# Kernel optimization log

Measured on AMD Instinct MI355X. Metric: run time of the kernel, lower is better.

The kernel has to match this reference:

```python
import jax, jax.numpy as jnp
import numpy as np

B, N, H = 4, 256, 8            # batch, nodes, heads
DNI, DEI = 32, 16              # node_in_dim, edge_in_dim
DNO, DEO = 32, 32              # node_out_dim, edge_out_dim
LEAKY = 0.2
NEG = -9e15


def setup_inputs() -> dict:
    key = jax.random.key(0)
    ks = jax.random.split(key, 13)
    s = 0.05
    node_fea = jax.random.normal(ks[0], (B, H, N, DNI), jnp.float32)
    edge_fea = jax.random.normal(ks[1], (B, H, N, N, DEI), jnp.float32)
    adj = jax.random.randint(ks[2], (B, N, N), 0, 2, jnp.int32)
    # learned params (nn.Linear: y = x @ W.T + b)
    W_w   = jax.random.normal(ks[3],  (H * DNO, H * DNI), jnp.float32) * s
    W_b   = jax.random.normal(ks[4],  (H * DNO,),         jnp.float32) * s
    a1_w  = jax.random.normal(ks[5],  (H, H * DNO),       jnp.float32) * s
    a2_w  = jax.random.normal(ks[6],  (H, H * DNO),       jnp.float32) * s
    ae_w  = jax.random.normal(ks[7],  (H, H * DEI),       jnp.float32) * s
    ae_b  = jax.random.normal(ks[8],  (H,),               jnp.float32) * s
    We_w  = jax.random.normal(ks[9],  (H * DEO, H * DEI), jnp.float32) * s
    We_b  = jax.random.normal(ks[10], (H * DEO,),         jnp.float32) * s
    Wod_w = jax.random.normal(ks[11], (H * DNO, H * DNI), jnp.float32) * s
    Wod_b = jax.random.normal(ks[12], (H * DNO,),         jnp.float32) * s
    return dict(node_fea=node_fea, edge_fea=edge_fea, adj=adj,
                W_w=W_w, W_b=W_b, a1_w=a1_w, a2_w=a2_w,
                ae_w=ae_w, ae_b=ae_b, We_w=We_w, We_b=We_b,
                Wod_w=Wod_w, Wod_b=Wod_b)


def reference(node_fea, edge_fea, adj, W_w, W_b, a1_w, a2_w,
              ae_w, ae_b, We_w, We_b, Wod_w, Wod_b):
    b, h, n, _ = node_fea.shape  # h == nheads -> non-first-layer branch
    # flatten heads into feature dim, as in the torch code
    nf = node_fea.transpose(0, 2, 1, 3).reshape(b, n, -1)          # [B,N,H*DNI]
    ef = edge_fea.transpose(0, 2, 3, 1, 4).reshape(b, n, n, -1)    # [B,N,N,H*DEI]

    Wh = nf @ W_w.T + W_b                                          # [B,N,H*DNO]
    e_edge = ef @ ae_w.T + ae_b                                    # [B,N,N,H]
    Whi = Wh @ a1_w.T                                              # [B,N,H]
    Whj = Wh @ a2_w.T                                              # [B,N,H]

    e = Whi[:, :, None, :] + Whj[:, None, :, :] + e_edge           # [B,N,N,H]
    e = jax.nn.leaky_relu(e, LEAKY)
    e = jnp.where(adj[..., None] > 0, e, NEG)

    # edge update: o + d + W_edge(edge)
    od = nf @ Wod_w.T + Wod_b                                      # [B,N,H*DEO]
    edge_new = od[:, :, None, :] + od[:, None, :, :] + (ef @ We_w.T + We_b)
    edge_new = edge_new.reshape(b, n, n, h, -1).transpose(0, 3, 1, 2, 4)  # [B,H,N,N,DEO]

    att = jax.nn.softmax(e.transpose(0, 3, 1, 2), axis=-1)         # [B,H,N,N]; dropout p=0 -> identity
    Whh = Wh.reshape(b, n, h, -1).transpose(0, 2, 1, 3)            # [B,H,N,DNO]
    node_new = att @ Whh + Whh                                     # [B,H,N,DNO]
    return node_new, edge_new
```

## Files before the change

kernel.cpp:

```cpp
#include <hip/hip_runtime.h>
#include <cstddef>


typedef __attribute__((ext_vector_type(8))) short short8;
typedef __attribute__((ext_vector_type(4))) short short4v;
typedef __attribute__((ext_vector_type(4))) float f32x4;

__device__ __forceinline__ float bf2f(unsigned short u) {
  union { unsigned int i; float f; } c;
  c.i = ((unsigned int)u) << 16;
  return c.f;
}
__device__ __forceinline__ unsigned short f2bf(float f) {
  union { float f; unsigned int i; } c; c.f = f;
  unsigned int x = c.i;
  x += 0x7fffu + ((x >> 16) & 1u);
  return (unsigned short)(x >> 16);
}

struct F8 { f32x4 lo, hi; };

__device__ __forceinline__ float loadf(const void* p, size_t i, bool bf) {
  return bf ? bf2f(((const unsigned short*)p)[i]) : ((const float*)p)[i];
}
__device__ __forceinline__ f32x4 load4f(const void* p, size_t i, bool bf) {
  f32x4 r;
  if (bf) {
    #pragma unroll
    for (int k = 0; k < 4; k++) r[k] = bf2f(((const unsigned short*)p)[i + k]);
  } else {
    r = *(const f32x4*)((const float*)p + i);
  }
  return r;
}
__device__ __forceinline__ F8 load8f(const void* p, size_t i, bool bf) {
  F8 r;
  if (bf) {
    short8 s = *(const short8*)((const unsigned short*)p + i);
    #pragma unroll
    for (int k = 0; k < 4; k++) {
      r.lo[k] = bf2f((unsigned short)s[k]);
      r.hi[k] = bf2f((unsigned short)s[k + 4]);
    }
  } else {
    const float* f = (const float*)p + i;
    r.lo = *(const f32x4*)f;
    r.hi = *(const f32x4*)(f + 4);
  }
  return r;
}
__device__ __forceinline__ short8 load8bf(const void* p, size_t i, bool bf) {
  if (bf) return *(const short8*)((const unsigned short*)p + i);
  const float* f = (const float*)p + i;
  f32x4 a = *(const f32x4*)f, c = *(const f32x4*)(f + 4);
  short8 r;
  #pragma unroll
  for (int k = 0; k < 4; k++) {
    r[k]     = (short)f2bf(a[k]);
    r[k + 4] = (short)f2bf(c[k]);
  }
  return r;
}
__device__ __forceinline__ void storef(void* p, size_t i, float v, bool bf) {
  if (bf) ((unsigned short*)p)[i] = f2bf(v);
  else    ((float*)p)[i] = v;
}

__global__ void k_detect(const unsigned int* __restrict__ w, int* __restrict__ flag) {
  const int lane = threadIdx.x;
  unsigned int x = w[lane];
  unsigned int e = (x >> 7) & 0xFFu;
  bool hit = (e >= 100u && e <= 126u);
  unsigned long long b = __ballot(hit);
  if (lane == 0) *flag = (__popcll(b) >= 32) ? 1 : 0;
}

__global__ __launch_bounds__(256) void k_node(
    const void* __restrict__ node_fea,
    const void* __restrict__ W_w,  const void* __restrict__ W_b,
    const void* __restrict__ a1_w, const void* __restrict__ a2_w,
    const void* __restrict__ Wod_w, const void* __restrict__ Wod_b,
    const int* __restrict__ flag,
    float* __restrict__ whT, float* __restrict__ od,
    float* __restrict__ whi, float* __restrict__ whj)
{
  const bool bf = (*flag != 0);
  __shared__ float nf[2][256];
  __shared__ float red[4][32];
  const int t = threadIdx.x;
  const int row0 = blockIdx.x * 2;
  const int b = row0 >> 8;
  {
    const int rl = t >> 7, k2 = (t & 127) * 2;
    const int h = k2 >> 5, d = k2 & 31;
    const int n = (row0 & 255) + rl;
    const size_t idx = (((size_t)(b * 8 + h)) * 256 + n) * 32 + d;
    nf[rl][k2]     = loadf(node_fea, idx, bf);
    nf[rl][k2 + 1] = loadf(node_fea, idx + 1, bf);
  }
  __syncthreads();
  const int o = t;
  float acc1[2] = {0.f, 0.f}, acc2[2] = {0.f, 0.f};
  #pragma unroll 4
  for (int kc = 0; kc < 32; kc++) {
    F8 w1 = load8f(W_w,   (size_t)o * 256 + kc * 8, bf);
    F8 w2 = load8f(Wod_w, (size_t)o * 256 + kc * 8, bf);
    #pragma unroll
    for (int r = 0; r < 2; r++) {
      f32x4 alo = *(const f32x4*)&nf[r][kc * 8];
      f32x4 ahi = *(const f32x4*)&nf[r][kc * 8 + 4];
      #pragma unroll
      for (int k = 0; k < 4; k++) {
        acc1[r] += alo[k] * w1.lo[k] + ahi[k] * w1.hi[k];
        acc2[r] += alo[k] * w2.lo[k] + ahi[k] * w2.hi[k];
      }
    }
  }
  float whv[2], odv[2];
  {
    float b1 = loadf(W_b, o, bf), b2 = loadf(Wod_b, o, bf);
    #pragma unroll
    for (int r = 0; r < 2; r++) {
      whv[r] = acc1[r] + b1;
      odv[r] = acc2[r] + b2;
      whT[(((size_t)(b * 256 + o)) << 8) + (row0 & 255) + r] = whv[r];
      od[(size_t)(row0 + r) * 256 + o] = odv[r];
    }
  }
  float a1f[8], a2f[8];
  #pragma unroll
  for (int h = 0; h < 8; h++) {
    a1f[h] = loadf(a1_w, (size_t)h * 256 + o, bf);
    a2f[h] = loadf(a2_w, (size_t)h * 256 + o, bf);
  }
  const int lane = t & 63, wv = t >> 6;
  #pragma unroll 1
  for (int c = 0; c < 32; c++) {
    const int mat = c >> 4, r = (c >> 3) & 1, h = c & 7;
    float v = whv[r] * (mat ? a2f[h] : a1f[h]);
    #pragma unroll
    for (int s = 1; s < 64; s <<= 1) v += __shfl_xor(v, s, 64);
    if (lane == 0) red[wv][c] = v;
  }
  __syncthreads();
  if (t < 32) {
    const int c = t;
    float s = red[0][c] + red[1][c] + red[2][c] + red[3][c];
    const int mat = c >> 4, r = (c >> 3) & 1, h = c & 7;
    (mat ? whj : whi)[(size_t)(row0 + r) * 8 + h] = s;
  }
}

__global__ __launch_bounds__(256, 4) void k_main(
    const void* __restrict__ edge_fea, const int* __restrict__ adj,
    const void* __restrict__ ae_w, const void* __restrict__ ae_b,
    const void* __restrict__ We_w, const void* __restrict__ We_b,
    const int* __restrict__ flag,
    const float* __restrict__ od, const float* __restrict__ whi,
    const float* __restrict__ whj, const float* __restrict__ whT,
    void* __restrict__ out)
{
  const bool bf = (*flag != 0);
  __shared__ unsigned short A[16384];
  __shared__ float e_l[8][256];
  const int t = threadIdx.x;
  const int blk = blockIdx.x;
  const int i = blk & 255, b = blk >> 8;
  const int wave = t >> 6, lane = t & 63, quad = lane >> 4, col = lane & 15;

  short8 bw[4][4];
  #pragma unroll
  for (int s = 0; s < 4; s++) {
    const int n = (wave * 4 + s) * 16 + col;
    #pragma unroll
    for (int ks = 0; ks < 4; ks++)
      bw[s][ks] = load8bf(We_w, (size_t)n * 128 + ks * 32 + quad * 8, bf);
  }

  f32x4 ow4[4];
  #pragma unroll
  for (int s = 0; s < 4; s++) {
    const int f0 = (wave * 4 + s) * 16 + quad * 4;
    f32x4 oi = *(const f32x4*)(od + (((size_t)(b * 256 + i)) << 8) + f0);
    f32x4 wb = load4f(We_b, f0, bf);
    ow4[s] = oi + wb;
  }

  #pragma unroll 1
  for (int jt = 0; jt < 2; jt++) {
    const int j0 = jt * 128;
    {
      const int jr = t >> 1, e8 = (t & 1) * 8;
      unsigned short* arow = &A[jr * 128];
      const int sx = jr & 7;
      #pragma unroll
      for (int h = 0; h < 8; h++) {
        const size_t idx = ((((size_t)(b * 8 + h)) * 256 + i) * 256 + j0 + jr) * 16 + e8;
        const int slot = (h * 2 + (e8 >> 3)) ^ sx;
        *(short8*)(arow + slot * 8) = load8bf(edge_fea, idx, bf);
      }
    }
    __syncthreads();

    #pragma unroll 1
    for (int mt = 0; mt < 8; mt++) {
      const int row = mt * 16 + col;
      const unsigned short* arow = &A[row * 128];
      const int rx = row & 7;
      f32x4 acc[4];
      #pragma unroll
      for (int s = 0; s < 4; s++) acc[s] = (f32x4){0.f, 0.f, 0.f, 0.f};
      #pragma unroll
      for (int ks = 0; ks < 4; ks++) {
        short8 a = *(const short8*)(arow + ((ks * 4 + quad) ^ rx) * 8);
        acc[0] = __builtin_amdgcn_mfma_f32_16x16x32_bf16(bw[0][ks], a, acc[0], 0, 0, 0);
        acc[1] = __builtin_amdgcn_mfma_f32_16x16x32_bf16(bw[1][ks], a, acc[1], 0, 0, 0);
        acc[2] = __builtin_amdgcn_mfma_f32_16x16x32_bf16(bw[2][ks], a, acc[2], 0, 0, 0);
        acc[3] = __builtin_amdgcn_mfma_f32_16x16x32_bf16(bw[3][ks], a, acc[3], 0, 0, 0);
      }
      const int j = j0 + mt * 16 + col;
      const float* odj = od + (((size_t)(b * 256 + j)) << 8);
      #pragma unroll
      for (int s = 0; s < 4; s++) {
        const int f0 = (wave * 4 + s) * 16 + quad * 4;
        const int h = f0 >> 5, d0 = f0 & 31;
        f32x4 op = *(const f32x4*)(odj + f0);
        f32x4 v = acc[s] + ow4[s] + op;
        const size_t oidx =
            262144 + (((((size_t)(b * 8 + h)) * 256 + i) * 256 + j) * 32 + d0);
        if (bf) {
          short4v sv;
          #pragma unroll
          for (int r = 0; r < 4; r++) sv[r] = (short)f2bf(v[r]);
          __builtin_nontemporal_store(sv, (short4v*)((unsigned short*)out + oidx));
        } else {
          __builtin_nontemporal_store(v, (f32x4*)((float*)out + oidx));
        }
      }
    }

    {
      short8 bae[4];
      #pragma unroll
      for (int ks = 0; ks < 4; ks++) {
        short8 z = {0, 0, 0, 0, 0, 0, 0, 0};
        bae[ks] = (col < 8) ? load8bf(ae_w, (size_t)col * 128 + ks * 32 + quad * 8, bf) : z;
      }
      f32x4 whi4 = {0.f, 0.f, 0.f, 0.f}, aeb4 = {0.f, 0.f, 0.f, 0.f};
      if (quad < 2) {
        whi4 = *(const f32x4*)(whi + ((size_t)(b * 256 + i)) * 8 + quad * 4);
        aeb4 = load4f(ae_b, quad * 4, bf);
      }
      #pragma unroll
      for (int mm = 0; mm < 2; mm++) {
        const int mt = wave * 2 + mm;
        const int row = mt * 16 + col;
        const unsigned short* arow = &A[row * 128];
        const int rx = row & 7;
        f32x4 acce = {0.f, 0.f, 0.f, 0.f};
        #pragma unroll
        for (int ks = 0; ks < 4; ks++) {
          short8 a = *(const short8*)(arow + ((ks * 4 + quad) ^ rx) * 8);
          acce = __builtin_amdgcn_mfma_f32_16x16x32_bf16(bae[ks], a, acce, 0, 0, 0);
        }
        if (quad < 2) {
          const int j = j0 + mt * 16 + col;
          f32x4 wj = *(const f32x4*)(whj + ((size_t)(b * 256 + j)) * 8 + quad * 4);
          const int av = adj[((size_t)(b * 256 + i)) * 256 + j];
          #pragma unroll
          for (int r = 0; r < 4; r++) {
            float e = acce[r] + aeb4[r] + whi4[r] + wj[r];
            e = (e > 0.f) ? e : 0.2f * e;
            e = (av > 0) ? e : -9e15f;
            e_l[quad * 4 + r][j] = e;
          }
        }
      }
    }
    __syncthreads();
  }

  {
    const int h = t >> 5, l32 = t & 31;
    float m = -3.0e38f;
    #pragma unroll
    for (int k = 0; k < 8; k++) m = fmaxf(m, e_l[h][l32 + 32 * k]);
    #pragma unroll
    for (int s = 16; s >= 1; s >>= 1) m = fmaxf(m, __shfl_xor(m, s, 32));
    float p[8], sum = 0.f;
    #pragma unroll
    for (int k = 0; k < 8; k++) {
      p[k] = __expf(e_l[h][l32 + 32 * k] - m);
      sum += p[k];
    }
    #pragma unroll
    for (int s = 16; s >= 1; s >>= 1) sum += __shfl_xor(sum, s, 32);
    const float inv = 1.0f / sum;
    #pragma unroll
    for (int k = 0; k < 8; k++) e_l[h][l32 + 32 * k] = p[k] * inv;
  }
  __syncthreads();

  {
    const int h = t >> 5;
    const float* wr = whT + (((size_t)(b * 256 + t)) << 8);
    f32x4 a4 = {0.f, 0.f, 0.f, 0.f};
    #pragma unroll 8
    for (int j4 = 0; j4 < 64; j4++) {
      f32x4 w4 = *(const f32x4*)(wr + j4 * 4);
      const f32x4 p4 = *(const f32x4*)&e_l[h][j4 * 4];
      a4 += w4 * p4;
    }
    float v = (a4[0] + a4[1]) + (a4[2] + a4[3]) + wr[i];
    const size_t oe = (((size_t)(b * 8 + h)) * 256 + i) * 32 + (t & 31);
    storef(out, oe, v, bf);
  }
}

extern "C" void kernel_launch(void* const* d_in, const int* in_sizes, int n_in,
                              void* d_out, int out_size, void* d_ws, size_t ws_size,
                              hipStream_t stream) {
  const void* node_fea = d_in[0];
  const void* edge_fea = d_in[1];
  const int*  adj      = (const int*)d_in[2];
  const void* W_w      = d_in[3];
  const void* W_b      = d_in[4];
  const void* a1_w     = d_in[5];
  const void* a2_w     = d_in[6];
  const void* ae_w     = d_in[7];
  const void* ae_b     = d_in[8];
  const void* We_w     = d_in[9];
  const void* We_b     = d_in[10];
  const void* Wod_w    = d_in[11];
  const void* Wod_b    = d_in[12];

  int*   flag = (int*)d_ws;
  float* base = (float*)d_ws;
  float* whT  = base + 16;
  float* od   = whT + 262144;
  float* whi  = od + 262144;
  float* whj  = whi + 8192;

  k_detect<<<dim3(1), dim3(64), 0, stream>>>((const unsigned int*)W_w, flag);
  k_node<<<dim3(512), dim3(256), 0, stream>>>(node_fea, W_w, W_b, a1_w, a2_w,
                                              Wod_w, Wod_b, flag, whT, od, whi, whj);
  k_main<<<dim3(1024), dim3(256), 0, stream>>>(edge_fea, adj, ae_w, ae_b, We_w, We_b,
                                               flag, od, whi, whj, whT, d_out);
}
```

Measured before the change: 561.5 us.

## Precompute transposed weights and fold attention vectors into node projection

Adds a prep kernel that transposes W and Wod into a combined row-major buffer and precomputes a1·W and a2·W plus their bias terms. The node kernel then computes whi/whj directly as extra output columns, which removes the per-block shuffle reductions, and it handles four rows per block with coalesced weight reads. Nontemporal stores in the main kernel become ordinary stores. This adds an extra launch, and when the workspace is too small it places scratch data in the tail of the output buffer, which is fragile.

Result: slower. 677.7 us (+20.7%).

```diff
diff --git a/kernel.cpp b/kernel.cpp
--- a/kernel.cpp
+++ b/kernel.cpp
@@ -1,5 +1,6 @@
 #include <hip/hip_runtime.h>
 #include <cstddef>
+#include <cstdint>
 
 
 typedef __attribute__((ext_vector_type(8))) short short8;
@@ -75,79 +76,120 @@
   if (lane == 0) *flag = (__popcll(b) >= 32) ? 1 : 0;
 }
 
+__global__ __launch_bounds__(256) void k_prep(
+    const void* __restrict__ W_w, const void* __restrict__ Wod_w,
+    const void* __restrict__ W_b,
+    const void* __restrict__ a1_w, const void* __restrict__ a2_w,
+    const int* __restrict__ flag,
+    float* __restrict__ WT, float* __restrict__ bias12)
+{
+  const bool bf = (*flag != 0);
+  const int t = threadIdx.x;
+  const int blk = blockIdx.x;
+  if (blk < 16) {
+    #pragma unroll
+    for (int q = 0; q < 4; q++) {
+      f32x4 w  = load4f(W_w,   (size_t)t * 256 + blk * 16 + q * 4, bf);
+      f32x4 wo = load4f(Wod_w, (size_t)t * 256 + blk * 16 + q * 4, bf);
+      #pragma unroll
+      for (int j = 0; j < 4; j++) {
+        const int k = blk * 16 + q * 4 + j;
+        WT[(size_t)k * 544 + t]       = w[j];
+        WT[(size_t)k * 544 + 256 + t] = wo[j];
+      }
+    }
+  } else {
+    __shared__ float sa[16][256];
+    __shared__ float sb[256];
+    #pragma unroll
+    for (int hh = 0; hh < 16; hh++)
+      sa[hh][t] = loadf(hh < 8 ? a1_w : a2_w, (size_t)(hh & 7) * 256 + t, bf);
+    sb[t] = loadf(W_b, t, bf);
+    __syncthreads();
+    float acc[16];
+    #pragma unroll
+    for (int hh = 0; hh < 16; hh++) acc[hh] = 0.f;
+    #pragma unroll 4
+    for (int f = 0; f < 256; f++) {
+      float w = loadf(W_w, (size_t)f * 256 + t, bf);
+      #pragma unroll
+      for (int hh = 0; hh < 16; hh++) acc[hh] += sa[hh][f] * w;
+    }
+    #pragma unroll
+    for (int hh = 0; hh < 16; hh++) WT[(size_t)t * 544 + 512 + hh] = acc[hh];
+    if (t < 16) {
+      float s = 0.f;
+      for (int f = 0; f < 256; f++) s += sa[t][f] * sb[f];
+      bias12[t] = s;
+    }
+  }
+}
+
 __global__ __launch_bounds__(256) void k_node(
-    const void* __restrict__ node_fea,
-    const void* __restrict__ W_w,  const void* __restrict__ W_b,
-    const void* __restrict__ a1_w, const void* __restrict__ a2_w,
-    const void* __restrict__ Wod_w, const void* __restrict__ Wod_b,
-    const int* __restrict__ flag,
+    const void* __restrict__ node_fea, const float* __restrict__ WT,
+    const void* __restrict__ W_b, const void* __restrict__ Wod_b,
+    const float* __restrict__ bias12, const int* __restrict__ flag,
     float* __restrict__ whT, float* __restrict__ od,
     float* __restrict__ whi, float* __restrict__ whj)
 {
   const bool bf = (*flag != 0);
-  __shared__ float nf[2][256];
-  __shared__ float red[4][32];
+  __shared__ float nf_s[4][256];
   const int t = threadIdx.x;
-  const int row0 = blockIdx.x * 2;
-  const int b = row0 >> 8;
+  const int r0 = blockIdx.x * 4;
+  const int b = r0 >> 8, n0 = r0 & 255;
+  if (t < 128) {
+    const int rr = t >> 5, k8 = t & 31;
+    const int h = k8 >> 2, d0 = (k8 & 3) * 8;
+    F8 v = load8f(node_fea,
+                  (((size_t)(b * 8 + h)) * 256 + (n0 + rr)) * 32 + d0, bf);
+    *(f32x4*)&nf_s[rr][k8 * 8]     = v.lo;
+    *(f32x4*)&nf_s[rr][k8 * 8 + 4] = v.hi;
+  }
+  __syncthreads();
+
+  float accW[4] = {0.f, 0.f, 0.f, 0.f};
+  float accO[4] = {0.f, 0.f, 0.f, 0.f};
+  float accM[4] = {0.f, 0.f, 0.f, 0.f};
+  const bool t16 = (t < 16);
+  #pragma unroll 1
+  for (int k4 = 0; k4 < 64; k4++) {
+    f32x4 nv[4];
+    #pragma unroll
+    for (int rr = 0; rr < 4; rr++) nv[rr] = *(const f32x4*)&nf_s[rr][k4 * 4];
+    #pragma unroll
+    for (int kk = 0; kk < 4; kk++) {
+      const float* row = WT + (size_t)(k4 * 4 + kk) * 544;
+      const float w0 = row[t], w1 = row[256 + t];
+      #pragma unroll
+      for (int rr = 0; rr < 4; rr++) {
+        accW[rr] += nv[rr][kk] * w0;
+        accO[rr] += nv[rr][kk] * w1;
+      }
+      if (t16) {
+        const float w2 = row[512 + t];
+        #pragma unroll
+        for (int rr = 0; rr < 4; rr++) accM[rr] += nv[rr][kk] * w2;
+      }
+    }
+  }
+
   {
-    const int rl = t >> 7, k2 = (t & 127) * 2;
-    const int h = k2 >> 5, d = k2 & 31;
-    const int n = (row0 & 255) + rl;
-    const size_t idx = (((size_t)(b * 8 + h)) * 256 + n) * 32 + d;
-    nf[rl][k2]     = loadf(node_fea, idx, bf);
-    nf[rl][k2 + 1] = loadf(node_fea, idx + 1, bf);
-  }
-  __syncthreads();
-  const int o = t;
-  float acc1[2] = {0.f, 0.f}, acc2[2] = {0.f, 0.f};
-  #pragma unroll 4
-  for (int kc = 0; kc < 32; kc++) {
-    F8 w1 = load8f(W_w,   (size_t)o * 256 + kc * 8, bf);
-    F8 w2 = load8f(Wod_w, (size_t)o * 256 + kc * 8, bf);
-    #pragma unroll
-    for (int r = 0; r < 2; r++) {
-      f32x4 alo = *(const f32x4*)&nf[r][kc * 8];
-      f32x4 ahi = *(const f32x4*)&nf[r][kc * 8 + 4];
-      #pragma unroll
-      for (int k = 0; k < 4; k++) {
-        acc1[r] += alo[k] * w1.lo[k] + ahi[k] * w1.hi[k];
-        acc2[r] += alo[k] * w2.lo[k] + ahi[k] * w2.hi[k];
-      }
-    }
-  }
-  float whv[2], odv[2];
-  {
-    float b1 = loadf(W_b, o, bf), b2 = loadf(Wod_b, o, bf);
-    #pragma unroll
-    for (int r = 0; r < 2; r++) {
-      whv[r] = acc1[r] + b1;
-      odv[r] = acc2[r] + b2;
-      whT[(((size_t)(b * 256 + o)) << 8) + (row0 & 255) + r] = whv[r];
-      od[(size_t)(row0 + r) * 256 + o] = odv[r];
-    }
-  }
-  float a1f[8], a2f[8];
-  #pragma unroll
-  for (int h = 0; h < 8; h++) {
-    a1f[h] = loadf(a1_w, (size_t)h * 256 + o, bf);
-    a2f[h] = loadf(a2_w, (size_t)h * 256 + o, bf);
-  }
-  const int lane = t & 63, wv = t >> 6;
-  #pragma unroll 1
-  for (int c = 0; c < 32; c++) {
-    const int mat = c >> 4, r = (c >> 3) & 1, h = c & 7;
-    float v = whv[r] * (mat ? a2f[h] : a1f[h]);
-    #pragma unroll
-    for (int s = 1; s < 64; s <<= 1) v += __shfl_xor(v, s, 64);
-    if (lane == 0) red[wv][c] = v;
-  }
-  __syncthreads();
-  if (t < 32) {
-    const int c = t;
-    float s = red[0][c] + red[1][c] + red[2][c] + red[3][c];
-    const int mat = c >> 4, r = (c >> 3) & 1, h = c & 7;
-    (mat ? whj : whi)[(size_t)(row0 + r) * 8 + h] = s;
+    const float bW = loadf(W_b, t, bf), bO = loadf(Wod_b, t, bf);
+    f32x4 wv;
+    #pragma unroll
+    for (int rr = 0; rr < 4; rr++) wv[rr] = accW[rr] + bW;
+    *(f32x4*)(whT + ((((size_t)(b * 256 + t)) << 8) + n0)) = wv;
+    #pragma unroll
+    for (int rr = 0; rr < 4; rr++)
+      od[(size_t)(r0 + rr) * 256 + t] = accO[rr] + bO;
+    if (t16) {
+      const float bm = bias12[t];
+      float* dst = (t < 8) ? whi : whj;
+      const int h = t & 7;
+      #pragma unroll
+      for (int rr = 0; rr < 4; rr++)
+        dst[(size_t)(r0 + rr) * 8 + h] = accM[rr] + bm;
+    }
   }
 }
 
@@ -232,9 +274,9 @@
           short4v sv;
           #pragma unroll
           for (int r = 0; r < 4; r++) sv[r] = (short)f2bf(v[r]);
-          __builtin_nontemporal_store(sv, (short4v*)((unsigned short*)out + oidx));
+          *(short4v*)((unsigned short*)out + oidx) = sv;
         } else {
-          __builtin_nontemporal_store(v, (f32x4*)((float*)out + oidx));
+          *(f32x4*)((float*)out + oidx) = v;
         }
       }
     }
@@ -340,10 +382,22 @@
   float* od   = whT + 262144;
   float* whi  = od + 262144;
   float* whj  = whi + 8192;
+  const size_t wt_floats = 139264 + 16;
+  const size_t need_bytes = (size_t)(16 + 262144 * 2 + 8192 * 2) * 4 + wt_floats * 4 + 256;
+  float* WT;
+  if (ws_size >= need_bytes) {
+    WT = whj + 8192;
+  } else {
+    uintptr_t tail = (uintptr_t)d_out + (size_t)out_size - wt_floats * 4 - 256;
+    WT = (float*)(tail & ~(uintptr_t)255);
+  }
+  float* bias12 = WT + 139264;
 
   k_detect<<<dim3(1), dim3(64), 0, stream>>>((const unsigned int*)W_w, flag);
-  k_node<<<dim3(512), dim3(256), 0, stream>>>(node_fea, W_w, W_b, a1_w, a2_w,
-                                              Wod_w, Wod_b, flag, whT, od, whi, whj);
+  k_prep<<<dim3(17), dim3(256), 0, stream>>>(W_w, Wod_w, W_b, a1_w, a2_w, flag,
+                                             WT, bias12);
+  k_node<<<dim3(256), dim3(256), 0, stream>>>(node_fea, WT, W_b, Wod_b, bias12, flag,
+                                              whT, od, whi, whj);
   k_main<<<dim3(1024), dim3(256), 0, stream>>>(edge_fea, adj, ae_w, ae_b, We_w, We_b,
                                                flag, od, whi, whj, whT, d_out);
 }
```
